# Performance work log

Hardware: AMD Instinct MI355X
Metric: run time of the kernel (lower is better)

Reference implementation:

```python
import jax, jax.numpy as jnp
import numpy as np

K = 16  # neighbors
LEAKY_SLOPE = 0.1  # CamLiFlow uses LeakyReLU(0.1)


def knn_indices(input_xyz, query_xyz, k):
    # input_xyz: [B,3,M], query_xyz: [B,3,N] -> [B,N,k] indices into M
    q = jnp.swapaxes(query_xyz, 1, 2)  # [B,N,3]
    p = jnp.swapaxes(input_xyz, 1, 2)  # [B,M,3]
    d2 = (jnp.sum(q * q, axis=-1)[:, :, None]
          + jnp.sum(p * p, axis=-1)[:, None, :]
          - 2.0 * jnp.einsum('bnc,bmc->bnm', q, p))  # [B,N,M]
    _, idx = jax.lax.top_k(-d2, k)
    return idx


def batch_indexing(x, idx):
    # x: [B,C,M], idx: [B,N,K] -> [B,C,N,K]
    return jax.vmap(lambda xb, ib: xb[:, ib])(x, idx)


def mlp2d(x, layers, act):
    # x: [B,C,N,K]; layers: list of (W[out,in], b[out]); 1x1 conv + act each layer
    for W, b in layers:
        x = act(jnp.einsum('oc,bcnk->bonk', W, x) + b[None, :, None, None])
    return x


def setup_inputs() -> dict:
    key = jax.random.key(0)
    B, N, CIN, COUT = 4, 8192, 64, 64
    ks = jax.random.split(key, 20)
    r = lambda k_, shp: jax.random.normal(k_, shp, dtype=jnp.float32) * 0.1
    return {
        'xyz1': jax.random.normal(ks[0], (B, 3, N), dtype=jnp.float32),
        'feat1': jax.random.normal(ks[1], (B, CIN, N), dtype=jnp.float32),
        'xyz2': jax.random.normal(ks[2], (B, 3, N), dtype=jnp.float32),
        'feat2': jax.random.normal(ks[3], (B, CIN, N), dtype=jnp.float32),
        'cost_w1': r(ks[4], (COUT, 3 + 2 * CIN)),
        'cost_b1': r(ks[5], (COUT,)),
        'cost_w2': r(ks[6], (COUT, COUT)),
        'cost_b2': r(ks[7], (COUT,)),
        'wn1_w1': r(ks[8], (8, 3)), 'wn1_b1': r(ks[9], (8,)),
        'wn1_w2': r(ks[10], (8, 8)), 'wn1_b2': r(ks[11], (8,)),
        'wn1_w3': r(ks[12], (COUT, 8)), 'wn1_b3': r(ks[13], (COUT,)),
        'wn2_w1': r(ks[14], (8, 3)), 'wn2_b1': r(ks[15], (8,)),
        'wn2_w2': r(ks[16], (8, 8)), 'wn2_b2': r(ks[17], (8,)),
        'wn2_w3': r(ks[18], (COUT, 8)), 'wn2_b3': r(ks[19], (COUT,)),
    }


def reference(xyz1, feat1, xyz2, feat2,
              cost_w1, cost_b1, cost_w2, cost_b2,
              wn1_w1, wn1_b1, wn1_w2, wn1_b2, wn1_w3, wn1_b3,
              wn2_w1, wn2_b1, wn2_w2, wn2_b2, wn2_w3, wn2_b3):
    B, Cin, N = feat1.shape
    leaky = lambda v: jax.nn.leaky_relu(v, LEAKY_SLOPE)
    relu = jax.nn.relu

    # Stage 1: point-to-point cost in cloud 2
    idx12 = knn_indices(xyz2, xyz1, K)                       # [B,N,K]
    knn_xyz2 = batch_indexing(xyz2, idx12)                   # [B,3,N,K]
    knn_xyz2_norm = knn_xyz2 - xyz1[:, :, :, None]           # [B,3,N,K]
    knn_feat2 = batch_indexing(feat2, idx12)                 # [B,Cin,N,K]
    feat1_exp = jnp.broadcast_to(feat1[:, :, :, None], (B, Cin, N, K))
    cat = jnp.concatenate([feat1_exp, knn_feat2, knn_xyz2_norm], axis=1)  # [B,2Cin+3,N,K]
    p2p_cost = mlp2d(cat, [(cost_w1, cost_b1), (cost_w2, cost_b2)], leaky)  # [B,Cout,N,K]
    weights2 = mlp2d(knn_xyz2_norm, [(wn2_w1, wn2_b1), (wn2_w2, wn2_b2), (wn2_w3, wn2_b3)], relu)
    p2n_cost = jnp.sum(weights2 * p2p_cost, axis=3)          # [B,Cout,N]

    # Stage 2: aggregate over neighbors in cloud 1
    idx11 = knn_indices(xyz1, xyz1, K)                       # [B,N,K]
    knn_xyz1 = batch_indexing(xyz1, idx11)
    knn_xyz1_norm = knn_xyz1 - xyz1[:, :, :, None]
    weights1 = mlp2d(knn_xyz1_norm, [(wn1_w1, wn1_b1), (wn1_w2, wn1_b2), (wn1_w3, wn1_b3)], relu)
    n2n_cost = batch_indexing(p2n_cost, idx11)               # [B,Cout,N,K]
    n2n_cost = jnp.sum(weights1 * n2n_cost, axis=3)          # [B,Cout,N]
    return n2n_cost  # feat_aligner is Identity (align_channels=None)
```

## Files before the change

### kernel.cpp

```cpp
#include <hip/hip_runtime.h>
#include <stdint.h>

#define BB 4
#define NN 8192
#define KK 16
#define BN (BB*NN)
#define BNK (BN*KK)

__global__ void k_xyzw(const float* __restrict__ xyz1, const float* __restrict__ xyz2,
                       float4* __restrict__ w1, float4* __restrict__ w2){
    int t = blockIdx.x*256 + threadIdx.x;
    if (t >= 2*BN) return;
    const float* src; float4* dst; int i;
    if (t < BN){ src = xyz1; dst = w1; i = t; }
    else       { src = xyz2; dst = w2; i = t - BN; }
    int b = i >> 13, m = i & (NN-1);
    const float* p = src + (size_t)b*3*NN + m;
    float x = p[0], y = p[NN], z = p[2*NN];
    dst[i] = make_float4(x, y, z, x*x + y*y + z*z);
}

__global__ __launch_bounds__(64) void k_prefeat(const float* __restrict__ feat,
                                                const float* __restrict__ W1,
                                                const float* __restrict__ bias, int colOff,
                                                float* __restrict__ out){
    __shared__ float Wt[64*64];
    __shared__ float bsh[64];
    int t = threadIdx.x;
    for (int ci = 0; ci < 64; ++ci)
        Wt[ci*64 + t] = W1[t*131 + colOff + ci];
    bsh[t] = bias ? bias[t] : 0.0f;
    __syncthreads();

    int col = blockIdx.x*64 + t;
    int b = col >> 13, n = col & (NN-1);
    const float* f = feat + (size_t)b*64*NN + n;
    float acc[64];
    #pragma unroll
    for (int co = 0; co < 64; ++co) acc[co] = 0.f;
    for (int ci = 0; ci < 64; ++ci){
        float v = f[(size_t)ci*NN];
        const float4* wrow = (const float4*)(Wt + ci*64);
        #pragma unroll
        for (int c4 = 0; c4 < 16; ++c4){
            float4 w = wrow[c4];
            acc[c4*4+0] = fmaf(w.x, v, acc[c4*4+0]);
            acc[c4*4+1] = fmaf(w.y, v, acc[c4*4+1]);
            acc[c4*4+2] = fmaf(w.z, v, acc[c4*4+2]);
            acc[c4*4+3] = fmaf(w.w, v, acc[c4*4+3]);
        }
    }
    float4* o = (float4*)(out + (size_t)col*64);
    const float4* bs = (const float4*)bsh;
    #pragma unroll
    for (int c4 = 0; c4 < 16; ++c4){
        float4 bb = bs[c4];
        o[c4] = make_float4(acc[c4*4+0]+bb.x, acc[c4*4+1]+bb.y,
                            acc[c4*4+2]+bb.z, acc[c4*4+3]+bb.w);
    }
}

#define SCAP 19
#define CHUNK 1024

__device__ __forceinline__ unsigned mono_f32(float f){
    unsigned u = __float_as_uint(f);
    return ((int)u >= 0) ? (u | 0x80000000u) : ~u;
}
__device__ __forceinline__ float unmono_f32(unsigned v){
    unsigned u = ((int)v < 0) ? (v & 0x7FFFFFFFu) : ~v;
    return __uint_as_float(u);
}
__device__ __forceinline__ unsigned long long mono_f64(double d){
    unsigned long long u = (unsigned long long)__double_as_longlong(d);
    return ((long long)u >= 0) ? (u | 0x8000000000000000ull) : ~u;
}
__device__ __forceinline__ double unmono_f64(unsigned long long v){
    unsigned long long u = ((long long)v < 0) ? (v & 0x7FFFFFFFFFFFFFFFull) : ~v;
    return __longlong_as_double((long long)u);
}

#define KSWAP(x,y) { unsigned long long _lo=(x), _hi=(y); bool _sw=_hi<_lo; (y)=_sw?_lo:_hi; (x)=_sw?_hi:_lo; }

#define INSERT_KEY(key)                                                     \
    if ((key) < A15){                                                       \
        A15 = (key);                                                        \
        KSWAP(A14,A15) KSWAP(A13,A14) KSWAP(A12,A13) KSWAP(A11,A12)         \
        KSWAP(A10,A11) KSWAP(A9,A10)  KSWAP(A8,A9)   KSWAP(A7,A8)           \
        KSWAP(A6,A7)   KSWAP(A5,A6)   KSWAP(A4,A5)   KSWAP(A3,A4)           \
        KSWAP(A2,A3)   KSWAP(A1,A2)   KSWAP(A0,A1)                          \
    }

#define FLUSH()                                                              \
    do {                                                                     \
        for (int s = 0; s < cnt; ++s){                                       \
            int j = stk[s];                                                  \
            float4 c = cb[j];                                                \
            double px = c.x, py = c.y, pz = c.z;                             \
            double pp  = fma(px,px, fma(py,py, pz*pz));                      \
            double dot = fma(qx,px, fma(qy,py, qz*pz));                      \
            double d2 = qq + pp - 2.0*dot;                                   \
            unsigned long long key =                                         \
                (mono_f64(d2) & ~8191ull) | (unsigned long long)(unsigned)j; \
            INSERT_KEY(key)                                                  \
        }                                                                    \
        cnt = 0;                                                             \
        float scr = (float)(unmono_f64(A15) - qq);                           \
        unsigned m = mono_f32(scr);                                          \
        unsigned old = atomicMin(&thrsh[lane], m);                           \
        bdt = unmono_f32(old < m ? old : m) + 1e-4f;                         \
    } while(0)

__global__ __launch_bounds__(512, 2) void k_knn(const float4* __restrict__ qpts,
                                             const float4* __restrict__ cA, const float4* __restrict__ cB,
                                             int* __restrict__ outA, int* __restrict__ outB){
    __shared__ unsigned int thrsh[64];
    __shared__ __align__(16) char pool[38912];

    const float4* cpts = (blockIdx.y == 0) ? cA : cB;
    int* out            = (blockIdx.y == 0) ? outA : outB;

    int tid = threadIdx.x;
    int lane = tid & 63;
    int wv = tid >> 6;
    int gq = blockIdx.x*64 + lane;
    int b = gq >> 13;
    float4 q = qpts[gq];
    float n2x = -2.f*q.x, n2y = -2.f*q.y, n2z = -2.f*q.z;
    double qx = q.x, qy = q.y, qz = q.z;
    double qq = fma(qx,qx, fma(qy,qy, qz*qz));

    if (tid < 64) thrsh[tid] = 0xFF800000u;
    __syncthreads();

    const unsigned long long KINIT = 0xFFF0000000000000ull | 8191ull;
    unsigned long long A0=KINIT, A1=KINIT, A2=KINIT, A3=KINIT,
                       A4=KINIT, A5=KINIT, A6=KINIT, A7=KINIT,
                       A8=KINIT, A9=KINIT, A10=KINIT, A11=KINIT,
                       A12=KINIT, A13=KINIT, A14=KINIT, A15=KINIT;

    float bdt = __builtin_inff();
    int cnt = 0;
    int* stk = ((int*)pool) + tid*SCAP;
    const float4* cb = cpts + (size_t)b*NN;

    int j0beg = wv*CHUNK;
    for (int jo = j0beg; jo < j0beg + CHUNK; jo += 128){
        {
            float f = unmono_f32(thrsh[lane]) + 1e-4f;
            bdt = fminf(bdt, f);
        }
        for (int j0 = jo; j0 < jo + 128; j0 += 4){
            const float4* cp = cb + j0;
            #pragma unroll
            for (int jj = 0; jj < 4; ++jj){
                float4 c = cp[jj];
                float t = fmaf(n2x, c.x, c.w);
                t = fmaf(n2y, c.y, t);
                t = fmaf(n2z, c.z, t);
                if (t < bdt){ stk[cnt] = j0 + jj; cnt++; }
            }
            if (__any(cnt >= 16)) FLUSH();
        }
    }
    FLUSH();

    __syncthreads();
    unsigned long long* mrg = (unsigned long long*)pool;
    #pragma unroll
    for (int r = 4; r >= 1; r >>= 1){
        if (wv >= r && wv < 2*r){
            unsigned long long* dst = mrg + ((size_t)(wv - r)*64 + lane)*17;
            dst[0]=A0;  dst[1]=A1;  dst[2]=A2;  dst[3]=A3;
            dst[4]=A4;  dst[5]=A5;  dst[6]=A6;  dst[7]=A7;
            dst[8]=A8;  dst[9]=A9;  dst[10]=A10; dst[11]=A11;
            dst[12]=A12; dst[13]=A13; dst[14]=A14; dst[15]=A15;
        }
        __syncthreads();
        if (wv < r){
            const unsigned long long* src = mrg + ((size_t)wv*64 + lane)*17;
            for (int i = 0; i < 16; ++i){
                unsigned long long bkey = src[i];
                if (__all(bkey >= A15)) break;
                INSERT_KEY(bkey)
            }
        }
        __syncthreads();
    }
    if (wv == 0){
        int4* o = (int4*)(out + (size_t)gq*16);
        o[0] = make_int4((int)(A0 & 8191ull),  (int)(A1 & 8191ull),
                         (int)(A2 & 8191ull),  (int)(A3 & 8191ull));
        o[1] = make_int4((int)(A4 & 8191ull),  (int)(A5 & 8191ull),
                         (int)(A6 & 8191ull),  (int)(A7 & 8191ull));
        o[2] = make_int4((int)(A8 & 8191ull),  (int)(A9 & 8191ull),
                         (int)(A10 & 8191ull), (int)(A11 & 8191ull));
        o[3] = make_int4((int)(A12 & 8191ull), (int)(A13 & 8191ull),
                         (int)(A14 & 8191ull), (int)(A15 & 8191ull));
    }
}

__global__ __launch_bounds__(256) void k_h2(const float4* __restrict__ qpts, const float4* __restrict__ cpts,
                                            const int* __restrict__ idx,
                                            const float* __restrict__ w1, const float* __restrict__ b1,
                                            const float* __restrict__ w2, const float* __restrict__ b2,
                                            float* __restrict__ H){
    int i = blockIdx.x*256 + threadIdx.x;
    int gq = i >> 4;
    int b = gq >> 13;
    int m = idx[i];
    float4 p = cpts[b*NN + m];
    float4 q = qpts[gq];
    float x = p.x - q.x, y = p.y - q.y, z = p.z - q.z;
    float h1[8], h2[8];
    #pragma unroll
    for (int j = 0; j < 8; ++j){
        float v = b1[j] + w1[j*3+0]*x + w1[j*3+1]*y + w1[j*3+2]*z;
        h1[j] = fmaxf(v, 0.f);
    }
    #pragma unroll
    for (int j = 0; j < 8; ++j){
        float v = b2[j];
        #pragma unroll
        for (int jj = 0; jj < 8; ++jj) v = fmaf(w2[j*8+jj], h1[jj], v);
        h2[j] = fmaxf(v, 0.f);
    }
    float4* o = (float4*)(H + (size_t)i*8);
    o[0] = make_float4(h2[0],h2[1],h2[2],h2[3]);
    o[1] = make_float4(h2[4],h2[5],h2[6],h2[7]);
}

__device__ __forceinline__ float rl_f(int hb, int lane_c){
    return __int_as_float(__builtin_amdgcn_readlane(hb, lane_c));
}

__global__ __launch_bounds__(256) void k_stage1(const float* __restrict__ A1, const float* __restrict__ A2,
                                                const int* __restrict__ idx12, const float* __restrict__ H12,
                                                const float4* __restrict__ xyzw1, const float4* __restrict__ xyzw2,
                                                const float* __restrict__ W1full, const float* __restrict__ W2,
                                                const float* __restrict__ b2, const float* __restrict__ w3,
                                                const float* __restrict__ b3, float* __restrict__ p2n){
    int lane = threadIdx.x & 63;
    int wv = threadIdx.x >> 6;
    int wgid = blockIdx.x*4 + wv;

    float w2r[64];
    const float4* w2p = (const float4*)(W2 + (size_t)lane*64);
    #pragma unroll
    for (int c4 = 0; c4 < 16; ++c4){
        float4 v = w2p[c4];
        w2r[c4*4+0]=v.x; w2r[c4*4+1]=v.y; w2r[c4*4+2]=v.z; w2r[c4*4+3]=v.w;
    }
    float w1cx = W1full[lane*131+128], w1cy = W1full[lane*131+129], w1cz = W1full[lane*131+130];
    float b2v = b2[lane], b3v = b3[lane];
    float w3r[8];
    {
        const float4* w3p = (const float4*)(w3 + (size_t)lane*8);
        float4 a = w3p[0], bq = w3p[1];
        w3r[0]=a.x; w3r[1]=a.y; w3r[2]=a.z; w3r[3]=a.w;
        w3r[4]=bq.x; w3r[5]=bq.y; w3r[6]=bq.z; w3r[7]=bq.w;
    }

    for (int task = wgid; task < BN; task += 4096){
        int b = task >> 13;
        float4 q = xyzw1[task];
        float a1 = A1[(size_t)task*64 + lane];
        float acc = 0.f;
        const int* ip = idx12 + (size_t)task*16;
        for (int k = 0; k < 16; ++k){
            int m = ip[k];
            float4 p = xyzw2[b*NN + m];
            float a2 = A2[(size_t)(b*NN+m)*64 + lane];
            float h = a1 + a2;
            h = fmaf(w1cx, p.x - q.x, h);
            h = fmaf(w1cy, p.y - q.y, h);
            h = fmaf(w1cz, p.z - q.z, h);
            h = fmaxf(h, 0.1f*h);
            int hb = __float_as_int(h);
            float c20 = 0.f, c21 = 0.f, c22 = 0.f, c23 = 0.f;
            #pragma unroll
            for (int c = 0; c < 64; c += 4){
                c20 = fmaf(w2r[c+0], rl_f(hb, c+0), c20);
                c21 = fmaf(w2r[c+1], rl_f(hb, c+1), c21);
                c22 = fmaf(w2r[c+2], rl_f(hb, c+2), c22);
                c23 = fmaf(w2r[c+3], rl_f(hb, c+3), c23);
            }
            float c2 = ((c20 + c21) + (c22 + c23)) + b2v;
            c2 = fmaxf(c2, 0.1f*c2);
            const float4* hw = (const float4*)(H12 + (size_t)(task*16+k)*8);
            float4 ha = hw[0], hb2 = hw[1];
            float w = b3v;
            w = fmaf(w3r[0], ha.x, w); w = fmaf(w3r[1], ha.y, w);
            w = fmaf(w3r[2], ha.z, w); w = fmaf(w3r[3], ha.w, w);
            w = fmaf(w3r[4], hb2.x, w); w = fmaf(w3r[5], hb2.y, w);
            w = fmaf(w3r[6], hb2.z, w); w = fmaf(w3r[7], hb2.w, w);
            w = fmaxf(w, 0.f);
            acc = fmaf(w, c2, acc);
        }
        p2n[(size_t)task*64 + lane] = acc;
    }
}

__global__ __launch_bounds__(256) void k_stage2(const float* __restrict__ p2n, const int* __restrict__ idx11,
                                                const float* __restrict__ H11, const float* __restrict__ w3,
                                                const float* __restrict__ b3, float* __restrict__ out){
    __shared__ float tl[64*65];
    int lane = threadIdx.x & 63;
    int wv = threadIdx.x >> 6;
    int base = blockIdx.x*64;
    int b = base >> 13;

    float w3r[8];
    {
        const float4* w3p = (const float4*)(w3 + (size_t)lane*8);
        float4 a = w3p[0], bq = w3p[1];
        w3r[0]=a.x; w3r[1]=a.y; w3r[2]=a.z; w3r[3]=a.w;
        w3r[4]=bq.x; w3r[5]=bq.y; w3r[6]=bq.z; w3r[7]=bq.w;
    }
    float b3v = b3[lane];

    for (int i = 0; i < 16; ++i){
        int col = base + wv*16 + i;
        const int* ip = idx11 + (size_t)col*16;
        const float* Hb = H11 + (size_t)col*16*8;
        float acc = 0.f;
        for (int k = 0; k < 16; ++k){
            int m = ip[k];
            float c = p2n[(size_t)(b*NN + m)*64 + lane];
            const float4* hw = (const float4*)(Hb + k*8);
            float4 ha = hw[0], hb2 = hw[1];
            float w = b3v;
            w = fmaf(w3r[0], ha.x, w);  w = fmaf(w3r[1], ha.y, w);
            w = fmaf(w3r[2], ha.z, w);  w = fmaf(w3r[3], ha.w, w);
            w = fmaf(w3r[4], hb2.x, w); w = fmaf(w3r[5], hb2.y, w);
            w = fmaf(w3r[6], hb2.z, w); w = fmaf(w3r[7], hb2.w, w);
            w = fmaxf(w, 0.f);
            acc = fmaf(w, c, acc);
        }
        tl[(wv*16+i)*65 + lane] = acc;
    }
    __syncthreads();
    int n0 = base & (NN-1);
    #pragma unroll
    for (int i = 0; i < 16; ++i){
        int co = i*4 + wv;
        float v = tl[lane*65 + co];
        out[((size_t)b*64 + co)*NN + n0 + lane] = v;
    }
}

extern "C" void kernel_launch(void* const* d_in, const int* in_sizes, int n_in,
                              void* d_out, int out_size, void* d_ws, size_t ws_size,
                              hipStream_t stream) {
    const float* xyz1   = (const float*)d_in[0];
    const float* feat1  = (const float*)d_in[1];
    const float* xyz2   = (const float*)d_in[2];
    const float* feat2  = (const float*)d_in[3];
    const float* cost_w1 = (const float*)d_in[4];
    const float* cost_b1 = (const float*)d_in[5];
    const float* cost_w2 = (const float*)d_in[6];
    const float* cost_b2 = (const float*)d_in[7];
    const float* wn1_w1 = (const float*)d_in[8];
    const float* wn1_b1 = (const float*)d_in[9];
    const float* wn1_w2 = (const float*)d_in[10];
    const float* wn1_b2 = (const float*)d_in[11];
    const float* wn1_w3 = (const float*)d_in[12];
    const float* wn1_b3 = (const float*)d_in[13];
    const float* wn2_w1 = (const float*)d_in[14];
    const float* wn2_b1 = (const float*)d_in[15];
    const float* wn2_w2 = (const float*)d_in[16];
    const float* wn2_b2 = (const float*)d_in[17];
    const float* wn2_w3 = (const float*)d_in[18];
    const float* wn2_b3 = (const float*)d_in[19];

    char* ws = (char*)d_ws;
    float4* xyzw1 = (float4*)(ws + 0);
    float4* xyzw2 = (float4*)(ws + 524288);
    float*  A1    = (float*)(ws + 1048576);
    float*  A2    = (float*)(ws + 9437184);
    int*    idx12 = (int*)  (ws + 17825792);
    int*    idx11 = (int*)  (ws + 19922944);
    float*  H12   = (float*)(ws + 22020096);
    float*  H11   = (float*)(ws + 38797312);
    float*  p2n   = (float*)(ws + 55574528);

    k_xyzw<<<256, 256, 0, stream>>>(xyz1, xyz2, xyzw1, xyzw2);
    k_prefeat<<<512, 64, 0, stream>>>(feat1, cost_w1, cost_b1, 0,  A1);
    k_prefeat<<<512, 64, 0, stream>>>(feat2, cost_w1, nullptr, 64, A2);
    k_knn<<<dim3(512,2), 512, 0, stream>>>(xyzw1, xyzw2, xyzw1, idx12, idx11);
    k_h2<<<2048, 256, 0, stream>>>(xyzw1, xyzw2, idx12, wn2_w1, wn2_b1, wn2_w2, wn2_b2, H12);
    k_h2<<<2048, 256, 0, stream>>>(xyzw1, xyzw1, idx11, wn1_w1, wn1_b1, wn1_w2, wn1_b2, H11);
    k_stage1<<<1024, 256, 0, stream>>>(A1, A2, idx12, H12, xyzw1, xyzw2,
                                       cost_w1, cost_w2, cost_b2, wn2_w3, wn2_b3, p2n);
    k_stage2<<<512, 256, 0, stream>>>(p2n, idx11, H11, wn1_w3, wn1_b3, (float*)d_out);
}
```

Measured before the change: 745.8 us.

## Add subsampled float prepass to seed the KNN pruning threshold

The KNN kernel now does a cheap float-only prepass over one of every four points in each wave's chunk. It keeps a register top-16 of the partial distances and publishes the 16th value as a shared per-query threshold through atomicMin. The full pass then starts with this tight bound, so far fewer candidates are pushed to the stack and refined in double precision. Because the subset's 16th-best is an upper bound on the true 16th-best, results stay exact. The cost is an extra partial scan, an extra barrier, and no further threshold sharing between waves during the main pass.

```diff
diff --git a/kernel.cpp b/kernel.cpp
--- a/kernel.cpp
+++ b/kernel.cpp
@@ -80,8 +80,17 @@
     return __longlong_as_double((long long)u);
 }
 
+#define FSWAP(x,y) { float _a = fminf((x),(y)), _b = fmaxf((x),(y)); (x)=_a; (y)=_b; }
+#define INSERT_F(t)                                                         \
+    if ((t) < T15){                                                         \
+        T15 = (t);                                                          \
+        FSWAP(T14,T15) FSWAP(T13,T14) FSWAP(T12,T13) FSWAP(T11,T12)         \
+        FSWAP(T10,T11) FSWAP(T9,T10)  FSWAP(T8,T9)   FSWAP(T7,T8)           \
+        FSWAP(T6,T7)   FSWAP(T5,T6)   FSWAP(T4,T5)   FSWAP(T3,T4)           \
+        FSWAP(T2,T3)   FSWAP(T1,T2)   FSWAP(T0,T1)                          \
+    }
+
 #define KSWAP(x,y) { unsigned long long _lo=(x), _hi=(y); bool _sw=_hi<_lo; (y)=_sw?_lo:_hi; (x)=_sw?_hi:_lo; }
-
 #define INSERT_KEY(key)                                                     \
     if ((key) < A15){                                                       \
         A15 = (key);                                                        \
@@ -90,26 +99,6 @@
         KSWAP(A6,A7)   KSWAP(A5,A6)   KSWAP(A4,A5)   KSWAP(A3,A4)           \
         KSWAP(A2,A3)   KSWAP(A1,A2)   KSWAP(A0,A1)                          \
     }
-
-#define FLUSH()                                                              \
-    do {                                                                     \
-        for (int s = 0; s < cnt; ++s){                                       \
-            int j = stk[s];                                                  \
-            float4 c = cb[j];                                                \
-            double px = c.x, py = c.y, pz = c.z;                             \
-            double pp  = fma(px,px, fma(py,py, pz*pz));                      \
-            double dot = fma(qx,px, fma(qy,py, qz*pz));                      \
-            double d2 = qq + pp - 2.0*dot;                                   \
-            unsigned long long key =                                         \
-                (mono_f64(d2) & ~8191ull) | (unsigned long long)(unsigned)j; \
-            INSERT_KEY(key)                                                  \
-        }                                                                    \
-        cnt = 0;                                                             \
-        float scr = (float)(unmono_f64(A15) - qq);                           \
-        unsigned m = mono_f32(scr);                                          \
-        unsigned old = atomicMin(&thrsh[lane], m);                           \
-        bdt = unmono_f32(old < m ? old : m) + 1e-4f;                         \
-    } while(0)
 
 __global__ __launch_bounds__(512, 2) void k_knn(const float4* __restrict__ qpts,
                                              const float4* __restrict__ cA, const float4* __restrict__ cB,
@@ -133,37 +122,80 @@
     if (tid < 64) thrsh[tid] = 0xFF800000u;
     __syncthreads();
 
-    const unsigned long long KINIT = 0xFFF0000000000000ull | 8191ull;
-    unsigned long long A0=KINIT, A1=KINIT, A2=KINIT, A3=KINIT,
-                       A4=KINIT, A5=KINIT, A6=KINIT, A7=KINIT,
-                       A8=KINIT, A9=KINIT, A10=KINIT, A11=KINIT,
-                       A12=KINIT, A13=KINIT, A14=KINIT, A15=KINIT;
-
-    float bdt = __builtin_inff();
+    const float4* cb = cpts + (size_t)b*NN;
+    int j0beg = wv*CHUNK;
     int cnt = 0;
-    int* stk = ((int*)pool) + tid*SCAP;
-    const float4* cb = cpts + (size_t)b*NN;
-
-    int j0beg = wv*CHUNK;
-    for (int jo = j0beg; jo < j0beg + CHUNK; jo += 128){
-        {
-            float f = unmono_f32(thrsh[lane]) + 1e-4f;
-            bdt = fminf(bdt, f);
-        }
-        for (int j0 = jo; j0 < jo + 128; j0 += 4){
-            const float4* cp = cb + j0;
+
+    {
+        float T0,T1,T2,T3,T4,T5,T6,T7,T8,T9,T10,T11,T12,T13,T14,T15;
+        const float FINF = __builtin_inff();
+        T0=FINF;T1=FINF;T2=FINF;T3=FINF;T4=FINF;T5=FINF;T6=FINF;T7=FINF;
+        T8=FINF;T9=FINF;T10=FINF;T11=FINF;T12=FINF;T13=FINF;T14=FINF;T15=FINF;
+        float bdtA = FINF;
+        float* stkf = ((float*)pool) + tid*SCAP;
+
+        for (int jo = j0beg; jo < j0beg + CHUNK; jo += 16){
+            const float4* cp = cb + jo;
             #pragma unroll
             for (int jj = 0; jj < 4; ++jj){
                 float4 c = cp[jj];
                 float t = fmaf(n2x, c.x, c.w);
                 t = fmaf(n2y, c.y, t);
                 t = fmaf(n2z, c.z, t);
-                if (t < bdt){ stk[cnt] = j0 + jj; cnt++; }
+                if (t < fminf(bdtA, T15)){ stkf[cnt] = t; cnt++; }
             }
-            if (__any(cnt >= 16)) FLUSH();
-        }
-    }
-    FLUSH();
+            if (__any(cnt >= 16)){
+                for (int s = 0; s < cnt; ++s){ float t = stkf[s]; INSERT_F(t) }
+                cnt = 0;
+                unsigned m = mono_f32(T15);
+                unsigned old = atomicMin(&thrsh[lane], m);
+                bdtA = unmono_f32(old < m ? old : m);
+            }
+        }
+        for (int s = 0; s < cnt; ++s){ float t = stkf[s]; INSERT_F(t) }
+        cnt = 0;
+        atomicMin(&thrsh[lane], mono_f32(T15));
+    }
+    __syncthreads();
+
+    const unsigned long long KINIT = 0xFFF0000000000000ull | 8191ull;
+    unsigned long long A0=KINIT, A1=KINIT, A2=KINIT, A3=KINIT,
+                       A4=KINIT, A5=KINIT, A6=KINIT, A7=KINIT,
+                       A8=KINIT, A9=KINIT, A10=KINIT, A11=KINIT,
+                       A12=KINIT, A13=KINIT, A14=KINIT, A15=KINIT;
+    float bdt = unmono_f32(thrsh[lane]) + 1e-4f;
+    int* stk = ((int*)pool) + tid*SCAP;
+
+    #define FLUSH_B()                                                            \
+        do {                                                                     \
+            for (int s = 0; s < cnt; ++s){                                       \
+                int j = stk[s];                                                  \
+                float4 c = cb[j];                                                \
+                double px = c.x, py = c.y, pz = c.z;                             \
+                double pp  = fma(px,px, fma(py,py, pz*pz));                      \
+                double dot = fma(qx,px, fma(qy,py, qz*pz));                      \
+                double d2 = qq + pp - 2.0*dot;                                   \
+                unsigned long long key =                                         \
+                    (mono_f64(d2) & ~8191ull) | (unsigned long long)(unsigned)j; \
+                INSERT_KEY(key)                                                  \
+            }                                                                    \
+            cnt = 0;                                                             \
+            bdt = fminf(bdt, (float)(unmono_f64(A15) - qq) + 1e-4f);             \
+        } while(0)
+
+    for (int j0 = j0beg; j0 < j0beg + CHUNK; j0 += 4){
+        const float4* cp = cb + j0;
+        #pragma unroll
+        for (int jj = 0; jj < 4; ++jj){
+            float4 c = cp[jj];
+            float t = fmaf(n2x, c.x, c.w);
+            t = fmaf(n2y, c.y, t);
+            t = fmaf(n2z, c.z, t);
+            if (t < bdt){ stk[cnt] = j0 + jj; cnt++; }
+        }
+        if (__any(cnt >= 16)) FLUSH_B();
+    }
+    FLUSH_B();
 
     __syncthreads();
     unsigned long long* mrg = (unsigned long long*)pool;
```

Measured after the change: 691.6 us. -7.3%, faster.

## Replace brute-force KNN with uniform grid binning and ring-expanding search

Applied to the files above, without the earlier changes.

Replaces the brute-force KNN kernel, which scanned all 8192 candidates per query, with a uniform 48^3 grid per batch and cloud. New kernels compute bounds, count per cell, prefix-scan, and scatter the points into cell-sorted order. A search kernel then visits shells of cells in growing rings around each query and stops once the shell's lower-bound distance exceeds the current 16th-best. This cuts distance evaluations sharply but adds several small kernels, atomics, and per-thread divergence. The workspace reuses the H12 region, which is safe only because H12 is written after the KNN kernel.

```diff
diff --git a/kernel.cpp b/kernel.cpp
--- a/kernel.cpp
+++ b/kernel.cpp
@@ -6,6 +6,10 @@
 #define KK 16
 #define BN (BB*NN)
 #define BNK (BN*KK)
+
+#define G   48
+#define G3  (G*G*G)
+#define G3P (G3+8)
 
 __global__ void k_xyzw(const float* __restrict__ xyz1, const float* __restrict__ xyz2,
                        float4* __restrict__ w1, float4* __restrict__ w2){
@@ -60,9 +64,6 @@
     }
 }
 
-#define SCAP 19
-#define CHUNK 1024
-
 __device__ __forceinline__ unsigned mono_f32(float f){
     unsigned u = __float_as_uint(f);
     return ((int)u >= 0) ? (u | 0x80000000u) : ~u;
@@ -80,8 +81,100 @@
     return __longlong_as_double((long long)u);
 }
 
+__device__ __forceinline__ void cell_of(float x, float y, float z,
+                                        const unsigned* bmin, const unsigned* bmax, int seg,
+                                        int& cx, int& cy, int& cz){
+    int s3 = seg*3;
+    float mnx = unmono_f32(bmin[s3+0]), mny = unmono_f32(bmin[s3+1]), mnz = unmono_f32(bmin[s3+2]);
+    float mxx = unmono_f32(bmax[s3+0]), mxy = unmono_f32(bmax[s3+1]), mxz = unmono_f32(bmax[s3+2]);
+    float ivx = (float)G/(mxx-mnx), ivy = (float)G/(mxy-mny), ivz = (float)G/(mxz-mnz);
+    cx = (int)((x-mnx)*ivx); cx = cx < 0 ? 0 : (cx > G-1 ? G-1 : cx);
+    cy = (int)((y-mny)*ivy); cy = cy < 0 ? 0 : (cy > G-1 ? G-1 : cy);
+    cz = (int)((z-mnz)*ivz); cz = cz < 0 ? 0 : (cz > G-1 ? G-1 : cz);
+}
+
+__global__ __launch_bounds__(256) void k_bounds(const float4* __restrict__ w1, const float4* __restrict__ w2,
+                                                unsigned* __restrict__ bmin, unsigned* __restrict__ bmax){
+    int t = blockIdx.x*256 + threadIdx.x;
+    int cloud = (t >= BN) ? 1 : 0;
+    int i = cloud ? t - BN : t;
+    float4 p = (cloud ? w2 : w1)[i];
+    float mn0 = p.x, mn1 = p.y, mn2 = p.z;
+    float mx0 = p.x, mx1 = p.y, mx2 = p.z;
+    #pragma unroll
+    for (int d = 1; d < 64; d <<= 1){
+        mn0 = fminf(mn0, __shfl_xor(mn0, d)); mx0 = fmaxf(mx0, __shfl_xor(mx0, d));
+        mn1 = fminf(mn1, __shfl_xor(mn1, d)); mx1 = fmaxf(mx1, __shfl_xor(mx1, d));
+        mn2 = fminf(mn2, __shfl_xor(mn2, d)); mx2 = fmaxf(mx2, __shfl_xor(mx2, d));
+    }
+    if ((threadIdx.x & 63) == 0){
+        int seg = cloud*4 + (i >> 13), s3 = seg*3;
+        atomicMin(&bmin[s3+0], mono_f32(mn0)); atomicMax(&bmax[s3+0], mono_f32(mx0));
+        atomicMin(&bmin[s3+1], mono_f32(mn1)); atomicMax(&bmax[s3+1], mono_f32(mx1));
+        atomicMin(&bmin[s3+2], mono_f32(mn2)); atomicMax(&bmax[s3+2], mono_f32(mx2));
+    }
+}
+
+__global__ __launch_bounds__(256) void k_count(const float4* __restrict__ w1, const float4* __restrict__ w2,
+                                               const unsigned* __restrict__ bmin, const unsigned* __restrict__ bmax,
+                                               int* __restrict__ counts){
+    int t = blockIdx.x*256 + threadIdx.x;
+    int cloud = (t >= BN) ? 1 : 0;
+    int i = cloud ? t - BN : t;
+    float4 p = (cloud ? w2 : w1)[i];
+    int seg = cloud*4 + (i >> 13);
+    int cx, cy, cz;
+    cell_of(p.x, p.y, p.z, bmin, bmax, seg, cx, cy, cz);
+    atomicAdd(&counts[seg*G3P + (cz*G + cy)*G + cx], 1);
+}
+
+__global__ __launch_bounds__(1024) void k_scan(const int* __restrict__ counts,
+                                               int* __restrict__ starts, int* __restrict__ offsets){
+    __shared__ int part[1024];
+    int seg = blockIdx.x;
+    const int* c = counts + (size_t)seg*G3P;
+    int* st = starts + (size_t)seg*G3P;
+    int* of = offsets + (size_t)seg*G3P;
+    int t = threadIdx.x;
+    int base = t*108;
+    int s = 0;
+    for (int i = 0; i < 108; ++i) s += c[base+i];
+    part[t] = s;
+    __syncthreads();
+    for (int d = 1; d < 1024; d <<= 1){
+        int add = (t >= d) ? part[t-d] : 0;
+        __syncthreads();
+        part[t] += add;
+        __syncthreads();
+    }
+    int run = part[t] - s;
+    for (int i = 0; i < 108; ++i){
+        st[base+i] = run;
+        of[base+i] = run;
+        run += c[base+i];
+    }
+    if (t == 1023) st[G3] = NN;
+}
+
+__global__ __launch_bounds__(256) void k_scatter(const float4* __restrict__ w1, const float4* __restrict__ w2,
+                                                 const unsigned* __restrict__ bmin, const unsigned* __restrict__ bmax,
+                                                 int* __restrict__ offsets,
+                                                 float4* __restrict__ sortedA, int* __restrict__ sortedIdx){
+    int t = blockIdx.x*256 + threadIdx.x;
+    int cloud = (t >= BN) ? 1 : 0;
+    int i = cloud ? t - BN : t;
+    float4 p = (cloud ? w2 : w1)[i];
+    int b = i >> 13;
+    int seg = cloud*4 + b;
+    int cx, cy, cz;
+    cell_of(p.x, p.y, p.z, bmin, bmax, seg, cx, cy, cz);
+    int pos = atomicAdd(&offsets[seg*G3P + (cz*G + cy)*G + cx], 1);
+    int dst = cloud*BN + b*NN + pos;
+    sortedA[dst] = p;
+    sortedIdx[dst] = i & (NN-1);
+}
+
 #define KSWAP(x,y) { unsigned long long _lo=(x), _hi=(y); bool _sw=_hi<_lo; (y)=_sw?_lo:_hi; (x)=_sw?_hi:_lo; }
-
 #define INSERT_KEY(key)                                                     \
     if ((key) < A15){                                                       \
         A15 = (key);                                                        \
@@ -91,113 +184,97 @@
         KSWAP(A2,A3)   KSWAP(A1,A2)   KSWAP(A0,A1)                          \
     }
 
-#define FLUSH()                                                              \
-    do {                                                                     \
-        for (int s = 0; s < cnt; ++s){                                       \
-            int j = stk[s];                                                  \
-            float4 c = cb[j];                                                \
-            double px = c.x, py = c.y, pz = c.z;                             \
-            double pp  = fma(px,px, fma(py,py, pz*pz));                      \
-            double dot = fma(qx,px, fma(qy,py, qz*pz));                      \
-            double d2 = qq + pp - 2.0*dot;                                   \
-            unsigned long long key =                                         \
-                (mono_f64(d2) & ~8191ull) | (unsigned long long)(unsigned)j; \
-            INSERT_KEY(key)                                                  \
-        }                                                                    \
-        cnt = 0;                                                             \
-        float scr = (float)(unmono_f64(A15) - qq);                           \
-        unsigned m = mono_f32(scr);                                          \
-        unsigned old = atomicMin(&thrsh[lane], m);                           \
-        bdt = unmono_f32(old < m ? old : m) + 1e-4f;                         \
-    } while(0)
-
-__global__ __launch_bounds__(512, 2) void k_knn(const float4* __restrict__ qpts,
-                                             const float4* __restrict__ cA, const float4* __restrict__ cB,
-                                             int* __restrict__ outA, int* __restrict__ outB){
-    __shared__ unsigned int thrsh[64];
-    __shared__ __align__(16) char pool[38912];
-
-    const float4* cpts = (blockIdx.y == 0) ? cA : cB;
-    int* out            = (blockIdx.y == 0) ? outA : outB;
-
-    int tid = threadIdx.x;
-    int lane = tid & 63;
-    int wv = tid >> 6;
-    int gq = blockIdx.x*64 + lane;
-    int b = gq >> 13;
-    float4 q = qpts[gq];
+__global__ __launch_bounds__(256) void k_knng(const float4* __restrict__ sortedA, const int* __restrict__ sortedIdx,
+                                              const int* __restrict__ starts,
+                                              const unsigned* __restrict__ bmin, const unsigned* __restrict__ bmax,
+                                              int* __restrict__ outA, int* __restrict__ outB){
+    int sp = blockIdx.x*256 + threadIdx.x;
+    int candCloud = (blockIdx.y == 0) ? 1 : 0;
+    int* out = (blockIdx.y == 0) ? outA : outB;
+    int b = sp >> 13;
+    float4 q = sortedA[sp];
+    int qorig = sortedIdx[sp];
+    int seg = candCloud*4 + b;
+
+    const float4* cA = sortedA + candCloud*BN + b*NN;
+    const int*    cI = sortedIdx + candCloud*BN + b*NN;
+    const int*    st = starts + (size_t)seg*G3P;
+
+    int s3 = seg*3;
+    float mnx = unmono_f32(bmin[s3+0]), mny = unmono_f32(bmin[s3+1]), mnz = unmono_f32(bmin[s3+2]);
+    float mxx = unmono_f32(bmax[s3+0]), mxy = unmono_f32(bmax[s3+1]), mxz = unmono_f32(bmax[s3+2]);
+    float hx = (mxx-mnx)*(1.f/G), hy = (mxy-mny)*(1.f/G), hz = (mxz-mnz)*(1.f/G);
+    float hmin = fminf(hx, fminf(hy, hz));
+    int cx, cy, cz;
+    cell_of(q.x, q.y, q.z, bmin, bmax, seg, cx, cy, cz);
+
     float n2x = -2.f*q.x, n2y = -2.f*q.y, n2z = -2.f*q.z;
+    float qq32 = q.w;
     double qx = q.x, qy = q.y, qz = q.z;
     double qq = fma(qx,qx, fma(qy,qy, qz*qz));
-
-    if (tid < 64) thrsh[tid] = 0xFF800000u;
-    __syncthreads();
 
     const unsigned long long KINIT = 0xFFF0000000000000ull | 8191ull;
     unsigned long long A0=KINIT, A1=KINIT, A2=KINIT, A3=KINIT,
                        A4=KINIT, A5=KINIT, A6=KINIT, A7=KINIT,
                        A8=KINIT, A9=KINIT, A10=KINIT, A11=KINIT,
                        A12=KINIT, A13=KINIT, A14=KINIT, A15=KINIT;
-
-    float bdt = __builtin_inff();
-    int cnt = 0;
-    int* stk = ((int*)pool) + tid*SCAP;
-    const float4* cb = cpts + (size_t)b*NN;
-
-    int j0beg = wv*CHUNK;
-    for (int jo = j0beg; jo < j0beg + CHUNK; jo += 128){
-        {
-            float f = unmono_f32(thrsh[lane]) + 1e-4f;
-            bdt = fminf(bdt, f);
-        }
-        for (int j0 = jo; j0 < jo + 128; j0 += 4){
-            const float4* cp = cb + j0;
-            #pragma unroll
-            for (int jj = 0; jj < 4; ++jj){
-                float4 c = cp[jj];
-                float t = fmaf(n2x, c.x, c.w);
-                t = fmaf(n2y, c.y, t);
-                t = fmaf(n2z, c.z, t);
-                if (t < bdt){ stk[cnt] = j0 + jj; cnt++; }
+    float d16a = __builtin_inff();
+    float thr  = __builtin_inff();
+
+    #define SCAN_RUN(c0, c1)                                                     \
+        { int _j0 = st[c0], _j1 = st[(c1)+1];                                    \
+          for (int j = _j0; j < _j1; ++j){                                       \
+              float4 cpt = cA[j];                                                \
+              float t = fmaf(n2x, cpt.x, cpt.w);                                 \
+              t = fmaf(n2y, cpt.y, t);                                           \
+              t = fmaf(n2z, cpt.z, t);                                           \
+              if (t < thr){                                                      \
+                  double px = cpt.x, py = cpt.y, pz = cpt.z;                     \
+                  double pp  = fma(px,px, fma(py,py, pz*pz));                    \
+                  double dot = fma(qx,px, fma(qy,py, qz*pz));                    \
+                  double d2 = qq + pp - 2.0*dot;                                 \
+                  unsigned long long key = (mono_f64(d2) & ~8191ull)             \
+                                         | (unsigned long long)(unsigned)cI[j];  \
+                  INSERT_KEY(key)                                                \
+                  d16a = fminf(d16a, (float)unmono_f64(A15));                    \
+                  thr  = d16a - qq32 + 1e-4f;                                    \
+              }                                                                  \
+          }                                                                      \
+        }
+
+    for (int r = 0; r < G; ++r){
+        if (r >= 1){
+            float lb = (float)(r-1) * hmin;
+            if (lb*lb*0.9998f - 1e-5f > d16a) break;
+        }
+        for (int dz = -r; dz <= r; ++dz){
+            int z = cz + dz; if ((unsigned)z >= (unsigned)G) continue;
+            for (int dy = -r; dy <= r; ++dy){
+                int y = cy + dy; if ((unsigned)y >= (unsigned)G) continue;
+                int rowbase = (z*G + y)*G;
+                bool edge = (dz == -r) || (dz == r) || (dy == -r) || (dy == r);
+                if (edge){
+                    int x0 = cx - r; if (x0 < 0) x0 = 0;
+                    int x1 = cx + r; if (x1 > G-1) x1 = G-1;
+                    SCAN_RUN(rowbase + x0, rowbase + x1)
+                } else {
+                    int xl = cx - r, xr = cx + r;
+                    if (xl >= 0)   SCAN_RUN(rowbase + xl, rowbase + xl)
+                    if (xr <= G-1) SCAN_RUN(rowbase + xr, rowbase + xr)
+                }
             }
-            if (__any(cnt >= 16)) FLUSH();
-        }
-    }
-    FLUSH();
-
-    __syncthreads();
-    unsigned long long* mrg = (unsigned long long*)pool;
-    #pragma unroll
-    for (int r = 4; r >= 1; r >>= 1){
-        if (wv >= r && wv < 2*r){
-            unsigned long long* dst = mrg + ((size_t)(wv - r)*64 + lane)*17;
-            dst[0]=A0;  dst[1]=A1;  dst[2]=A2;  dst[3]=A3;
-            dst[4]=A4;  dst[5]=A5;  dst[6]=A6;  dst[7]=A7;
-            dst[8]=A8;  dst[9]=A9;  dst[10]=A10; dst[11]=A11;
-            dst[12]=A12; dst[13]=A13; dst[14]=A14; dst[15]=A15;
-        }
-        __syncthreads();
-        if (wv < r){
-            const unsigned long long* src = mrg + ((size_t)wv*64 + lane)*17;
-            for (int i = 0; i < 16; ++i){
-                unsigned long long bkey = src[i];
-                if (__all(bkey >= A15)) break;
-                INSERT_KEY(bkey)
-            }
-        }
-        __syncthreads();
-    }
-    if (wv == 0){
-        int4* o = (int4*)(out + (size_t)gq*16);
-        o[0] = make_int4((int)(A0 & 8191ull),  (int)(A1 & 8191ull),
-                         (int)(A2 & 8191ull),  (int)(A3 & 8191ull));
-        o[1] = make_int4((int)(A4 & 8191ull),  (int)(A5 & 8191ull),
-                         (int)(A6 & 8191ull),  (int)(A7 & 8191ull));
-        o[2] = make_int4((int)(A8 & 8191ull),  (int)(A9 & 8191ull),
-                         (int)(A10 & 8191ull), (int)(A11 & 8191ull));
-        o[3] = make_int4((int)(A12 & 8191ull), (int)(A13 & 8191ull),
-                         (int)(A14 & 8191ull), (int)(A15 & 8191ull));
-    }
+        }
+    }
+
+    int4* o = (int4*)(out + ((size_t)(b*NN + qorig))*16);
+    o[0] = make_int4((int)(A0 & 8191ull),  (int)(A1 & 8191ull),
+                     (int)(A2 & 8191ull),  (int)(A3 & 8191ull));
+    o[1] = make_int4((int)(A4 & 8191ull),  (int)(A5 & 8191ull),
+                     (int)(A6 & 8191ull),  (int)(A7 & 8191ull));
+    o[2] = make_int4((int)(A8 & 8191ull),  (int)(A9 & 8191ull),
+                     (int)(A10 & 8191ull), (int)(A11 & 8191ull));
+    o[3] = make_int4((int)(A12 & 8191ull), (int)(A13 & 8191ull),
+                     (int)(A14 & 8191ull), (int)(A15 & 8191ull));
 }
 
 __global__ __launch_bounds__(256) void k_h2(const float4* __restrict__ qpts, const float4* __restrict__ cpts,
@@ -384,10 +461,27 @@
     float*  H11   = (float*)(ws + 38797312);
     float*  p2n   = (float*)(ws + 55574528);
 
+    char* g = ws + 22020096;
+    int*      counts    = (int*)     (g + 0);
+    int*      starts    = (int*)     (g + 3539200);
+    int*      offsets   = (int*)     (g + 7078400);
+    float4*   sortedA   = (float4*)  (g + 10617600);
+    int*      sortedIdx = (int*)     (g + 11666176);
+    unsigned* bmin      = (unsigned*)(g + 11928320);
+    unsigned* bmax      = (unsigned*)(g + 11928448);
+
+    hipMemsetAsync(counts, 0, (size_t)8*G3P*4, stream);
+    hipMemsetAsync(bmin, 0xFF, 96, stream);
+    hipMemsetAsync(bmax, 0x00, 96, stream);
+
     k_xyzw<<<256, 256, 0, stream>>>(xyz1, xyz2, xyzw1, xyzw2);
     k_prefeat<<<512, 64, 0, stream>>>(feat1, cost_w1, cost_b1, 0,  A1);
     k_prefeat<<<512, 64, 0, stream>>>(feat2, cost_w1, nullptr, 64, A2);
-    k_knn<<<dim3(512,2), 512, 0, stream>>>(xyzw1, xyzw2, xyzw1, idx12, idx11);
+    k_bounds<<<256, 256, 0, stream>>>(xyzw1, xyzw2, bmin, bmax);
+    k_count<<<256, 256, 0, stream>>>(xyzw1, xyzw2, bmin, bmax, counts);
+    k_scan<<<8, 1024, 0, stream>>>(counts, starts, offsets);
+    k_scatter<<<256, 256, 0, stream>>>(xyzw1, xyzw2, bmin, bmax, offsets, sortedA, sortedIdx);
+    k_knng<<<dim3(128, 2), 256, 0, stream>>>(sortedA, sortedIdx, starts, bmin, bmax, idx12, idx11);
     k_h2<<<2048, 256, 0, stream>>>(xyzw1, xyzw2, idx12, wn2_w1, wn2_b1, wn2_w2, wn2_b2, H12);
     k_h2<<<2048, 256, 0, stream>>>(xyzw1, xyzw1, idx11, wn1_w1, wn1_b1, wn1_w2, wn1_b2, H11);
     k_stage1<<<1024, 256, 0, stream>>>(A1, A2, idx12, H12, xyzw1, xyzw2,
```

Result: slower. 2.961 ms (+297.0%).
